# Performance work log

Hardware: AMD Instinct MI355X
Metric: run time of the kernel (lower is better)

Reference implementation:

```python
import jax, jax.numpy as jnp
import numpy as np

B, S, D, H = 1, 4096, 1024, 16
HD = D // H  # head_dim = 64
NEG = -1e9


def _rotate_half(x):
    x1, x2 = jnp.split(x, 2, axis=-1)
    return jnp.concatenate([-x2, x1], axis=-1)


def _apply_rope(x, cos, sin):
    # x: [b, s, h, hd]; cos/sin: [s, hd] -> broadcast over batch and heads
    c = cos[None, :, None, :]
    s = sin[None, :, None, :]
    return x * c + _rotate_half(x) * s


def setup_inputs() -> dict:
    key = jax.random.key(0)
    kx, kq, ko = jax.random.split(key, 3)
    x = jax.random.normal(kx, (B, S, D), dtype=jnp.float32)
    # causal additive mask (finite large-negative for safe grads)
    i = jnp.arange(S)
    attn_mask = jnp.where(i[None, :] > i[:, None], NEG, 0.0).astype(jnp.float32)[None, None]
    # standard RoPE tables
    inv_freq = 1.0 / (10000.0 ** (np.arange(0, HD, 2, dtype=np.float32) / HD))
    ang = np.arange(S, dtype=np.float32)[:, None] * inv_freq[None, :]  # [S, HD/2]
    ang = np.concatenate([ang, ang], axis=-1)  # [S, HD]
    rope_cos = jnp.asarray(np.cos(ang))
    rope_sin = jnp.asarray(np.sin(ang))
    W_qkv = jax.random.normal(kq, (D, 3 * D), dtype=jnp.float32) * (D ** -0.5)
    W_out = jax.random.normal(ko, (D, D), dtype=jnp.float32) * (D ** -0.5)
    return {"x": x, "attn_mask": attn_mask, "rope_cos": rope_cos,
            "rope_sin": rope_sin, "W_qkv": W_qkv, "W_out": W_out}


def reference(x, attn_mask, rope_cos, rope_sin, W_qkv, W_out):
    b, s, d = x.shape
    qkv = x @ W_qkv                              # [b, s, 3d]
    q, k, v = jnp.split(qkv, 3, axis=-1)
    q = q.reshape(b, s, H, HD)
    k = k.reshape(b, s, H, HD)
    v = v.reshape(b, s, H, HD)
    q = _apply_rope(q, rope_cos, rope_sin)
    k = _apply_rope(k, rope_cos, rope_sin)
    att = jnp.einsum('bqhd,bkhd->bhqk', q, k) / jnp.sqrt(jnp.float32(HD))
    att = att + attn_mask                        # additive mask broadcast [b,h,s,s]
    att = jax.nn.softmax(att, axis=-1)
    out = jnp.einsum('bhqk,bkhd->bqhd', att, v).reshape(b, s, d)
    return out @ W_out
```

## Files before the change

### kernel.cpp

```cpp
#include <hip/hip_runtime.h>


typedef __attribute__((ext_vector_type(8)))  __bf16 bf16x8;
typedef __attribute__((ext_vector_type(4)))  float  f32x4;
typedef __attribute__((ext_vector_type(16))) float  f32x16;
typedef __attribute__((ext_vector_type(8)))  unsigned short ushort8;
typedef __attribute__((ext_vector_type(4)))  unsigned int   u32x4;

#define MFMA16(a,b,c) __builtin_amdgcn_mfma_f32_16x16x32_bf16((a),(b),(c),0,0,0)
#define MFMA32(a,b,c) __builtin_amdgcn_mfma_f32_32x32x16_bf16((a),(b),(c),0,0,0)

static __device__ __forceinline__ unsigned short f2bf(float f) {
  unsigned int u = __builtin_bit_cast(unsigned int, f);
  u = (u + 0x7FFFu + ((u >> 16) & 1u)) >> 16;
  return (unsigned short)u;
}
static __device__ __forceinline__ float bf2f(unsigned short u) {
  return __builtin_bit_cast(float, (unsigned int)u << 16);
}
static __device__ __forceinline__ unsigned int cvtpk(float a, float b) {
  unsigned int r;
  asm("v_cvt_pk_bf16_f32 %0, %1, %2" : "=v"(r) : "v"(a), "v"(b));
  return r;
}
static __device__ __forceinline__ void plswap(unsigned int& a, unsigned int& b) {
#if __has_builtin(__builtin_amdgcn_permlane32_swap)
  auto r = __builtin_amdgcn_permlane32_swap(a, b, false, false);
  a = r[0]; b = r[1];
#else
  unsigned int xa = (unsigned int)__shfl_xor((int)a, 32);
  unsigned int xb = (unsigned int)__shfl_xor((int)b, 32);
  int lane = __builtin_amdgcn_mbcnt_hi(~0u, __builtin_amdgcn_mbcnt_lo(~0u, 0));
  bool hi = lane >= 32;
  a = hi ? xb : a;
  b = hi ? b : xa;
#endif
}

#if __has_builtin(__builtin_amdgcn_global_load_lds)
static __device__ __forceinline__ void STAGE16(const unsigned short* gp, const unsigned short* lp) {
  __builtin_amdgcn_global_load_lds(
      (const __attribute__((address_space(1))) void*)(unsigned long long)(uintptr_t)gp,
      (__attribute__((address_space(3))) void*)(unsigned int)(uintptr_t)lp,
      16, 0, 0);
}
static __device__ __forceinline__ void STAGE_WAIT() {  }
#else
static __device__ __forceinline__ void STAGE16(const unsigned short* gp, const unsigned short* lp) {
  unsigned int m0v = __builtin_amdgcn_readfirstlane((unsigned int)(unsigned long long)(uintptr_t)lp);
  asm volatile("s_mov_b32 m0, %0\n\tglobal_load_lds_dwordx4 %1, off"
               :: "s"(m0v), "v"(gp) : "memory");
}
static __device__ __forceinline__ void STAGE_WAIT() {
  asm volatile("s_waitcnt vmcnt(0)" ::: "memory");
}
#endif

__global__ __launch_bounds__(256) void prep_a(const float* __restrict__ x,
                                              const float* __restrict__ W_qkv,
                                              const float* __restrict__ W_out,
                                              unsigned short* __restrict__ xbf,
                                              unsigned short* __restrict__ WqkvT,
                                              unsigned short* __restrict__ WoutT) {
  __shared__ float t[32][33];
  int b = blockIdx.x, tid = threadIdx.x;
  if (b < 4096) {
    int i = (b * 256 + tid) * 4;
    float4 v = *reinterpret_cast<const float4*>(x + i);
    ushort4 u;
    u.x = f2bf(v.x); u.y = f2bf(v.y); u.z = f2bf(v.z); u.w = f2bf(v.w);
    *reinterpret_cast<ushort4*>(xbf + i) = u;
    return;
  }
  const float* W; unsigned short* WT; int R, C, cx, ry;
  if (b < 4096 + 3072) {
    int idx = b - 4096; W = W_qkv; WT = WqkvT; R = 1024; C = 3072;
    cx = idx % 96; ry = idx / 96;
  } else {
    int idx = b - 7168; W = W_out; WT = WoutT; R = 1024; C = 1024;
    cx = idx % 32; ry = idx / 32;
  }
  int c0 = cx * 32, r0 = ry * 32;
  int tx = tid & 31, ty = tid >> 5;
#pragma unroll
  for (int i = 0; i < 32; i += 8)
    t[ty + i][tx] = W[(size_t)(r0 + ty + i) * C + c0 + tx];
  __syncthreads();
#pragma unroll
  for (int i = 0; i < 32; i += 8)
    WT[(size_t)(c0 + ty + i) * R + r0 + tx] = f2bf(t[tx][ty + i]);
}

template <typename OutT>
__global__ __launch_bounds__(256) void gemm_lds(const unsigned short* __restrict__ A,
                                                const unsigned short* __restrict__ BT,
                                                OutT* __restrict__ C, int M, int N, int K) {
  __shared__ __align__(16) unsigned short As[128 * 32];
  __shared__ __align__(16) unsigned short Bs[128 * 32];
  int tid = threadIdx.x;
  int lane = tid & 63, w = tid >> 6;
  int wr = w >> 1, wc = w & 1;
  int row0 = blockIdx.y * 128, col0 = blockIdx.x * 128;
  int lr = lane & 15, lk = lane >> 4;
  int slk = (lk ^ ((lr >> 1) & 3)) * 8;
  int c0i = tid,        r0i = c0i >> 2, cs0 = ((c0i & 3) ^ ((r0i >> 1) & 3)) * 8;
  int c1i = 256 + tid,  r1i = c1i >> 2, cs1 = ((c1i & 3) ^ ((r1i >> 1) & 3)) * 8;
  const unsigned short* dA0 = &As[w * 512];
  const unsigned short* dB0 = &Bs[w * 512];
  const unsigned short* dA1 = &As[2048 + w * 512];
  const unsigned short* dB1 = &Bs[2048 + w * 512];
  const unsigned short* sA0 = A  + (size_t)(row0 + r0i) * K + cs0;
  const unsigned short* sB0 = BT + (size_t)(col0 + r0i) * K + cs0;
  const unsigned short* sA1 = A  + (size_t)(row0 + r1i) * K + cs1;
  const unsigned short* sB1 = BT + (size_t)(col0 + r1i) * K + cs1;
  f32x4 acc[4][4] = {};
  for (int k0 = 0; k0 < K; k0 += 32) {
    STAGE16(sA0 + k0, dA0);
    STAGE16(sB0 + k0, dB0);
    STAGE16(sA1 + k0, dA1);
    STAGE16(sB1 + k0, dB1);
    STAGE_WAIT();
    __syncthreads();
    bf16x8 a[4], b[4];
#pragma unroll
    for (int m = 0; m < 4; m++)
      a[m] = *reinterpret_cast<const bf16x8*>(&As[(wr * 64 + m * 16 + lr) * 32 + slk]);
#pragma unroll
    for (int n = 0; n < 4; n++)
      b[n] = *reinterpret_cast<const bf16x8*>(&Bs[(wc * 64 + n * 16 + lr) * 32 + slk]);
#pragma unroll
    for (int m = 0; m < 4; m++)
#pragma unroll
      for (int n = 0; n < 4; n++)
        acc[m][n] = MFMA16(a[m], b[n], acc[m][n]);
    __syncthreads();
  }
#pragma unroll
  for (int m = 0; m < 4; m++)
#pragma unroll
    for (int n = 0; n < 4; n++)
#pragma unroll
      for (int r = 0; r < 4; r++) {
        size_t off = (size_t)(row0 + wr * 64 + m * 16 + lk * 4 + r) * N + col0 + wc * 64 + n * 16 + lr;
        if constexpr (sizeof(OutT) == 2) C[off] = f2bf(acc[m][n][r]);
        else                             C[off] = acc[m][n][r];
      }
}

__global__ __launch_bounds__(256) void prep_b(const unsigned short* __restrict__ qkv,
                                              const float* __restrict__ cosb,
                                              const float* __restrict__ sinb,
                                              unsigned short* __restrict__ Q,
                                              unsigned short* __restrict__ K,
                                              unsigned short* __restrict__ VF) {
  __shared__ unsigned short tile[32][68];
  int b = blockIdx.x, tid = threadIdx.x;
  if (b < 2048) {
    const float QSCALE = 0.125f * 1.4426950408889634f;
    int idx = b * 256 + tid;
    int c = idx & 7, s = (idx >> 3) & 4095, h = idx >> 15;
    int d0 = c * 8;
    int base = s * 3072 + h * 64;
    ushort8 qv  = *reinterpret_cast<const ushort8*>(qkv + base + d0);
    ushort8 qv2 = *reinterpret_cast<const ushort8*>(qkv + base + (d0 ^ 32));
    ushort8 kv  = *reinterpret_cast<const ushort8*>(qkv + base + 1024 + d0);
    ushort8 kv2 = *reinterpret_cast<const ushort8*>(qkv + base + 1024 + (d0 ^ 32));
    float sign = (d0 < 32) ? -1.f : 1.f;
    const float4* cp = reinterpret_cast<const float4*>(cosb + s * 64 + d0);
    const float4* sp = reinterpret_cast<const float4*>(sinb + s * 64 + d0);
    float4 c0 = cp[0], c1 = cp[1], s0 = sp[0], s1 = sp[1];
    float co[8] = {c0.x, c0.y, c0.z, c0.w, c1.x, c1.y, c1.z, c1.w};
    float si[8] = {s0.x, s0.y, s0.z, s0.w, s1.x, s1.y, s1.z, s1.w};
    ushort8 qo, ko;
#pragma unroll
    for (int j = 0; j < 8; ++j) {
      float q = bf2f(qv[j]), q2 = bf2f(qv2[j]);
      float k = bf2f(kv[j]), k2 = bf2f(kv2[j]);
      qo[j] = f2bf((q * co[j] + sign * q2 * si[j]) * QSCALE);
      ko[j] = f2bf(k * co[j] + sign * k2 * si[j]);
    }
    *reinterpret_cast<ushort8*>(Q + (size_t)h * 262144 + (size_t)s * 64 + d0) = qo;
    int tt = s >> 5, ql = s & 31, lo = (d0 >> 3) & 1, f = d0 >> 4;
    size_t koff = (size_t)h * 262144 + (size_t)tt * 2048 + (size_t)f * 512
                + (size_t)(lo * 32 + ql) * 8;
    *reinterpret_cast<ushort8*>(K + koff) = ko;
    return;
  }
  int vb = b - 2048;
  int t = vb & 127, h = vb >> 7;
  {
    int r = tid >> 3, c8 = (tid & 7) * 8;
    *reinterpret_cast<ushort8*>(&tile[r][c8]) =
        *reinterpret_cast<const ushort8*>(qkv + (size_t)(t * 32 + r) * 3072 + 2048 + h * 64 + c8);
  }
  __syncthreads();
  int f = tid >> 6, lane = tid & 63;
  int ql = lane & 31, lo = lane >> 5;
  int sb = (f & 1) * 16 + lo * 8;
  int d  = (f >> 1) * 32 + ql;
  ushort8 v;
#pragma unroll
  for (int j = 0; j < 8; ++j) v[j] = tile[sb + j][d];
  *reinterpret_cast<ushort8*>(VF + (size_t)h * 262144 + (size_t)t * 2048
                              + (size_t)f * 512 + (size_t)lane * 8) = v;
}

__global__ __launch_bounds__(512) void flash_attn4q(const unsigned short* __restrict__ Q,
                                                    const unsigned short* __restrict__ Kf,
                                                    const unsigned short* __restrict__ Vf,
                                                    unsigned short* __restrict__ O) {
  const int S = 4096;
  __shared__ __align__(16) unsigned short sbuf[2][4][2048];
  int flat = blockIdx.x;
  int xcd = flat & 7;
  int r = flat >> 3;
  int h2 = r >> 5, rb = r & 31;
  int h = xcd * 2 + h2;
  int b = h2 ? (31 - rb) : rb;
  int nwin = (98 + b) >> 1;
  int tid = threadIdx.x;
  int lane = tid & 63, w = tid >> 6;
  int qm = w >> 1, pp = w & 1;
  int img = w >> 1, half = w & 1;
  int ql = lane & 31, lo = lane >> 5;
  const unsigned short* Qh  = Q  + (size_t)h * S * 64;
  const unsigned short* KfH = Kf + (size_t)h * S * 64;
  const unsigned short* VfH = Vf + (size_t)h * S * 64;
  const unsigned short* img_src = (img & 1) ? VfH : KfH;
  int img_dt = img >> 1;

  auto stage = [&](int nb, int win) {
    int t = 2 * win + img_dt;
    const unsigned short* src = img_src + (size_t)t * 2048 + half * 1024 + lane * 8;
    const unsigned short* dst = &sbuf[nb][img][half * 1024];
    STAGE16(src, dst);
    STAGE16(src + 512, dst + 512);
  };

  int qt = b + 32 * qm;
  int q0 = qt * 32;
  bf16x8 qf[4];
#pragma unroll
  for (int f = 0; f < 4; ++f)
    qf[f] = *reinterpret_cast<const bf16x8*>(Qh + (q0 + ql) * 64 + f * 16 + lo * 8);
  f32x16 oT0 = {}, oT1 = {};
  float l = 0.f;

  stage(0, 0);
  STAGE_WAIT();
  __syncthreads();
  int cb = 0;
  for (int win = 0; win < nwin; ++win) {
    if (win + 1 < nwin) stage(cb ^ 1, win + 1);
    int t = 2 * win + pp;
    if (t <= qt) {
      const unsigned short* kb = &sbuf[cb][2 * pp][0];
      const unsigned short* vb = &sbuf[cb][2 * pp + 1][0];
      bf16x8 k0 = *reinterpret_cast<const bf16x8*>(kb + 0 * 512 + lane * 8);
      bf16x8 k1 = *reinterpret_cast<const bf16x8*>(kb + 1 * 512 + lane * 8);
      bf16x8 k2 = *reinterpret_cast<const bf16x8*>(kb + 2 * 512 + lane * 8);
      bf16x8 k3 = *reinterpret_cast<const bf16x8*>(kb + 3 * 512 + lane * 8);
      f32x16 p = {};
      __builtin_amdgcn_s_setprio(1);
      p = MFMA32(k0, qf[0], p);
      p = MFMA32(k1, qf[1], p);
      p = MFMA32(k2, qf[2], p);
      p = MFMA32(k3, qf[3], p);
      __builtin_amdgcn_s_setprio(0);
      bf16x8 v00 = *reinterpret_cast<const bf16x8*>(vb + 0 * 512 + lane * 8);
      bf16x8 v01 = *reinterpret_cast<const bf16x8*>(vb + 1 * 512 + lane * 8);
      bf16x8 v10 = *reinterpret_cast<const bf16x8*>(vb + 2 * 512 + lane * 8);
      bf16x8 v11 = *reinterpret_cast<const bf16x8*>(vb + 3 * 512 + lane * 8);
      if (t == qt) {
#pragma unroll
        for (int r2 = 0; r2 < 16; ++r2) {
          int kvr = (r2 & 3) + 8 * (r2 >> 2) + 4 * lo;
          if (kvr > ql) p[r2] = -1e9f;
        }
      }
#pragma unroll
      for (int r2 = 0; r2 < 16; ++r2) p[r2] = __builtin_amdgcn_exp2f(p[r2]);
      {
        float s0 = (p[0] + p[1])   + (p[2] + p[3]);
        float s1 = (p[4] + p[5])   + (p[6] + p[7]);
        float s2 = (p[8] + p[9])   + (p[10] + p[11]);
        float s3 = (p[12] + p[13]) + (p[14] + p[15]);
        l += (s0 + s1) + (s2 + s3);
      }
      unsigned int A0 = cvtpk(p[0],  p[1]),  A1 = cvtpk(p[2],  p[3]);
      unsigned int B0 = cvtpk(p[4],  p[5]),  B1 = cvtpk(p[6],  p[7]);
      plswap(A0, B0); plswap(A1, B1);
      u32x4 w0 = {A0, A1, B0, B1};
      bf16x8 P0 = __builtin_bit_cast(bf16x8, w0);
      unsigned int C0 = cvtpk(p[8],  p[9]),  C1 = cvtpk(p[10], p[11]);
      unsigned int D0 = cvtpk(p[12], p[13]), D1 = cvtpk(p[14], p[15]);
      plswap(C0, D0); plswap(C1, D1);
      u32x4 w1 = {C0, C1, D0, D1};
      bf16x8 P1 = __builtin_bit_cast(bf16x8, w1);
      __builtin_amdgcn_s_setprio(1);
      oT0 = MFMA32(v00, P0, oT0);
      oT1 = MFMA32(v10, P0, oT1);
      oT0 = MFMA32(v01, P1, oT0);
      oT1 = MFMA32(v11, P1, oT1);
      __builtin_amdgcn_s_setprio(0);
    }
    STAGE_WAIT();
    __syncthreads();
    cb ^= 1;
  }

  float* fm = reinterpret_cast<float*>(&sbuf[0][0][0]);
  float* lm = fm + 2 * 64 * 33;
#pragma unroll
  for (int sub = 0; sub < 2; ++sub) {
    __syncthreads();
    if ((qm >> 1) == sub && pp == 1) {
      float* dst = fm + ((qm & 1) * 64 + lane) * 33;
#pragma unroll
      for (int r2 = 0; r2 < 16; ++r2) { dst[r2] = oT0[r2]; dst[16 + r2] = oT1[r2]; }
      lm[(qm & 1) * 64 + lane] = l;
    }
    __syncthreads();
    if ((qm >> 1) == sub && pp == 0) {
      const float* src = fm + ((qm & 1) * 64 + lane) * 33;
      float ll = l + lm[(qm & 1) * 64 + lane];
#pragma unroll
      for (int r2 = 0; r2 < 16; ++r2) {
        oT0[r2] += src[r2];
        oT1[r2] += src[16 + r2];
      }
      ll += __shfl_xor(ll, 32);
      float rl = 1.0f / ll;
      size_t obase = (size_t)(q0 + ql) * 1024 + h * 64;
#pragma unroll
      for (int r2 = 0; r2 < 16; ++r2) {
        int d = (r2 & 3) + 8 * (r2 >> 2) + 4 * lo;
        O[obase + d]      = f2bf(oT0[r2] * rl);
        O[obase + 32 + d] = f2bf(oT1[r2] * rl);
      }
    }
  }
}

extern "C" void kernel_launch(void* const* d_in, const int* in_sizes, int n_in,
                              void* d_out, int out_size, void* d_ws, size_t ws_size,
                              hipStream_t stream) {
  const float* x        = (const float*)d_in[0];
  const float* rope_cos = (const float*)d_in[2];
  const float* rope_sin = (const float*)d_in[3];
  const float* W_qkv    = (const float*)d_in[4];
  const float* W_out    = (const float*)d_in[5];
  float* out = (float*)d_out;

  char* ws = (char*)d_ws;
  const size_t MB = 1u << 20;
  unsigned short* xbf   = (unsigned short*)(ws + 0 * MB);
  unsigned short* WqkvT = (unsigned short*)(ws + 8 * MB);
  unsigned short* WoutT = (unsigned short*)(ws + 14 * MB);
  unsigned short* qkv   = (unsigned short*)(ws + 16 * MB);
  unsigned short* Qb    = (unsigned short*)(ws + 40 * MB);
  unsigned short* Kfb   = (unsigned short*)(ws + 48 * MB);
  unsigned short* Vfb   = (unsigned short*)(ws + 56 * MB);
  unsigned short* Ob    = (unsigned short*)(ws + 64 * MB);

  prep_a<<<8192, 256, 0, stream>>>(x, W_qkv, W_out, xbf, WqkvT, WoutT);

  gemm_lds<unsigned short><<<dim3(3072 / 128, 4096 / 128), 256, 0, stream>>>(
      xbf, WqkvT, qkv, 4096, 3072, 1024);

  prep_b<<<4096, 256, 0, stream>>>(qkv, rope_cos, rope_sin, Qb, Kfb, Vfb);

  flash_attn4q<<<512, 512, 0, stream>>>(Qb, Kfb, Vfb, Ob);

  gemm_lds<float><<<dim3(1024 / 128, 4096 / 128), 256, 0, stream>>>(
      Ob, WoutT, out, 4096, 1024, 1024);
}
```

Baseline: 134.3 us.

## Assign contiguous query tiles per block and stage four KV tiles per round

Each block now handles four adjacent 32-row query tiles (4g..4g+3) instead of two far-apart tiles (b and b+32), and each round stages four K/V tiles into a doubled shared buffer. Each warp then processes two KV tiles per round. This halves the number of barrier-synchronised rounds per KV span and keeps the block's query tiles close, so masked-out work is small. The cost is twice the LDS footprint, which may reduce occupancy, and a different causal load balance across blocks, since round counts now range from 1 to 32.

Result: faster. 128.6 us (-4.3%).

```diff
diff --git a/kernel.cpp b/kernel.cpp
--- a/kernel.cpp
+++ b/kernel.cpp
@@ -210,34 +210,36 @@
                                                     const unsigned short* __restrict__ Vf,
                                                     unsigned short* __restrict__ O) {
   const int S = 4096;
-  __shared__ __align__(16) unsigned short sbuf[2][4][2048];
+  __shared__ __align__(16) unsigned short sbuf[2][8][2048];
   int flat = blockIdx.x;
   int xcd = flat & 7;
-  int r = flat >> 3;
-  int h2 = r >> 5, rb = r & 31;
+  int v = flat >> 3;
+  int h2 = v >> 5, gslot = v & 31;
   int h = xcd * 2 + h2;
-  int b = h2 ? (31 - rb) : rb;
-  int nwin = (98 + b) >> 1;
+  int g = h2 ? (31 - gslot) : gslot;
+  int base4 = 4 * g;
+  int nround = g + 1;
   int tid = threadIdx.x;
   int lane = tid & 63, w = tid >> 6;
   int qm = w >> 1, pp = w & 1;
-  int img = w >> 1, half = w & 1;
   int ql = lane & 31, lo = lane >> 5;
   const unsigned short* Qh  = Q  + (size_t)h * S * 64;
   const unsigned short* KfH = Kf + (size_t)h * S * 64;
   const unsigned short* VfH = Vf + (size_t)h * S * 64;
-  const unsigned short* img_src = (img & 1) ? VfH : KfH;
-  int img_dt = img >> 1;
-
-  auto stage = [&](int nb, int win) {
-    int t = 2 * win + img_dt;
-    const unsigned short* src = img_src + (size_t)t * 2048 + half * 1024 + lane * 8;
-    const unsigned short* dst = &sbuf[nb][img][half * 1024];
-    STAGE16(src, dst);
-    STAGE16(src + 512, dst + 512);
+  const unsigned short* img_src = (w & 1) ? VfH : KfH;
+  int img_dt = w >> 1;
+
+  auto stage = [&](int nb, int rnd) {
+    int t = 4 * rnd + img_dt;
+    const unsigned short* src = img_src + (size_t)t * 2048 + lane * 8;
+    const unsigned short* dst = &sbuf[nb][w][0];
+    STAGE16(src,        dst);
+    STAGE16(src + 512,  dst + 512);
+    STAGE16(src + 1024, dst + 1024);
+    STAGE16(src + 1536, dst + 1536);
   };
 
-  int qt = b + 32 * qm;
+  int qt = base4 + qm;
   int q0 = qt * 32;
   bf16x8 qf[4];
 #pragma unroll
@@ -250,59 +252,63 @@
   STAGE_WAIT();
   __syncthreads();
   int cb = 0;
-  for (int win = 0; win < nwin; ++win) {
-    if (win + 1 < nwin) stage(cb ^ 1, win + 1);
-    int t = 2 * win + pp;
-    if (t <= qt) {
-      const unsigned short* kb = &sbuf[cb][2 * pp][0];
-      const unsigned short* vb = &sbuf[cb][2 * pp + 1][0];
-      bf16x8 k0 = *reinterpret_cast<const bf16x8*>(kb + 0 * 512 + lane * 8);
-      bf16x8 k1 = *reinterpret_cast<const bf16x8*>(kb + 1 * 512 + lane * 8);
-      bf16x8 k2 = *reinterpret_cast<const bf16x8*>(kb + 2 * 512 + lane * 8);
-      bf16x8 k3 = *reinterpret_cast<const bf16x8*>(kb + 3 * 512 + lane * 8);
-      f32x16 p = {};
-      __builtin_amdgcn_s_setprio(1);
-      p = MFMA32(k0, qf[0], p);
-      p = MFMA32(k1, qf[1], p);
-      p = MFMA32(k2, qf[2], p);
-      p = MFMA32(k3, qf[3], p);
-      __builtin_amdgcn_s_setprio(0);
-      bf16x8 v00 = *reinterpret_cast<const bf16x8*>(vb + 0 * 512 + lane * 8);
-      bf16x8 v01 = *reinterpret_cast<const bf16x8*>(vb + 1 * 512 + lane * 8);
-      bf16x8 v10 = *reinterpret_cast<const bf16x8*>(vb + 2 * 512 + lane * 8);
-      bf16x8 v11 = *reinterpret_cast<const bf16x8*>(vb + 3 * 512 + lane * 8);
-      if (t == qt) {
-#pragma unroll
-        for (int r2 = 0; r2 < 16; ++r2) {
-          int kvr = (r2 & 3) + 8 * (r2 >> 2) + 4 * lo;
-          if (kvr > ql) p[r2] = -1e9f;
+  for (int rnd = 0; rnd < nround; ++rnd) {
+    if (rnd + 1 < nround) stage(cb ^ 1, rnd + 1);
+#pragma unroll
+    for (int sub = 0; sub < 2; ++sub) {
+      int t = 4 * rnd + 2 * sub + pp;
+      if (t <= qt) {
+        int dt = 2 * sub + pp;
+        const unsigned short* kb = &sbuf[cb][2 * dt][0];
+        const unsigned short* vb = &sbuf[cb][2 * dt + 1][0];
+        bf16x8 k0 = *reinterpret_cast<const bf16x8*>(kb + 0 * 512 + lane * 8);
+        bf16x8 k1 = *reinterpret_cast<const bf16x8*>(kb + 1 * 512 + lane * 8);
+        bf16x8 k2 = *reinterpret_cast<const bf16x8*>(kb + 2 * 512 + lane * 8);
+        bf16x8 k3 = *reinterpret_cast<const bf16x8*>(kb + 3 * 512 + lane * 8);
+        f32x16 p = {};
+        __builtin_amdgcn_s_setprio(1);
+        p = MFMA32(k0, qf[0], p);
+        p = MFMA32(k1, qf[1], p);
+        p = MFMA32(k2, qf[2], p);
+        p = MFMA32(k3, qf[3], p);
+        __builtin_amdgcn_s_setprio(0);
+        bf16x8 v00 = *reinterpret_cast<const bf16x8*>(vb + 0 * 512 + lane * 8);
+        bf16x8 v01 = *reinterpret_cast<const bf16x8*>(vb + 1 * 512 + lane * 8);
+        bf16x8 v10 = *reinterpret_cast<const bf16x8*>(vb + 2 * 512 + lane * 8);
+        bf16x8 v11 = *reinterpret_cast<const bf16x8*>(vb + 3 * 512 + lane * 8);
+        if (t == qt) {
+#pragma unroll
+          for (int r2 = 0; r2 < 16; ++r2) {
+            int kvr = (r2 & 3) + 8 * (r2 >> 2) + 4 * lo;
+            if (kvr > ql) p[r2] = -1e9f;
+          }
         }
+#pragma unroll
+        for (int r2 = 0; r2 < 16; ++r2) p[r2] = __builtin_amdgcn_exp2f(p[r2]);
+        {
+          float s0 = (p[0] + p[1])   + (p[2] + p[3]);
+          float s1 = (p[4] + p[5])   + (p[6] + p[7]);
+          float s2 = (p[8] + p[9])   + (p[10] + p[11]);
+          float s3 = (p[12] + p[13]) + (p[14] + p[15]);
+          l += (s0 + s1) + (s2 + s3);
+        }
+        unsigned int A0 = cvtpk(p[0],  p[1]),  A1 = cvtpk(p[2],  p[3]);
+        unsigned int B0 = cvtpk(p[4],  p[5]),  B1 = cvtpk(p[6],  p[7]);
+        plswap(A0, B0); plswap(A1, B1);
+        u32x4 w0 = {A0, A1, B0, B1};
+        bf16x8 P0 = __builtin_bit_cast(bf16x8, w0);
+        unsigned int C0 = cvtpk(p[8],  p[9]),  C1 = cvtpk(p[10], p[11]);
+        unsigned int D0 = cvtpk(p[12], p[13]), D1 = cvtpk(p[14], p[15]);
+        plswap(C0, D0); plswap(C1, D1);
+        u32x4 w1 = {C0, C1, D0, D1};
+        bf16x8 P1 = __builtin_bit_cast(bf16x8, w1);
+        __builtin_amdgcn_s_setprio(1);
+        oT0 = MFMA32(v00, P0, oT0);
+        oT1 = MFMA32(v10, P0, oT1);
+        oT0 = MFMA32(v01, P1, oT0);
+        oT1 = MFMA32(v11, P1, oT1);
+        __builtin_amdgcn_s_setprio(0);
       }
-#pragma unroll
-      for (int r2 = 0; r2 < 16; ++r2) p[r2] = __builtin_amdgcn_exp2f(p[r2]);
-      {
-        float s0 = (p[0] + p[1])   + (p[2] + p[3]);
-        float s1 = (p[4] + p[5])   + (p[6] + p[7]);
-        float s2 = (p[8] + p[9])   + (p[10] + p[11]);
-        float s3 = (p[12] + p[13]) + (p[14] + p[15]);
-        l += (s0 + s1) + (s2 + s3);
-      }
-      unsigned int A0 = cvtpk(p[0],  p[1]),  A1 = cvtpk(p[2],  p[3]);
-      unsigned int B0 = cvtpk(p[4],  p[5]),  B1 = cvtpk(p[6],  p[7]);
-      plswap(A0, B0); plswap(A1, B1);
-      u32x4 w0 = {A0, A1, B0, B1};
-      bf16x8 P0 = __builtin_bit_cast(bf16x8, w0);
-      unsigned int C0 = cvtpk(p[8],  p[9]),  C1 = cvtpk(p[10], p[11]);
-      unsigned int D0 = cvtpk(p[12], p[13]), D1 = cvtpk(p[14], p[15]);
-      plswap(C0, D0); plswap(C1, D1);
-      u32x4 w1 = {C0, C1, D0, D1};
-      bf16x8 P1 = __builtin_bit_cast(bf16x8, w1);
-      __builtin_amdgcn_s_setprio(1);
-      oT0 = MFMA32(v00, P0, oT0);
-      oT1 = MFMA32(v10, P0, oT1);
-      oT0 = MFMA32(v01, P1, oT0);
-      oT1 = MFMA32(v11, P1, oT1);
-      __builtin_amdgcn_s_setprio(0);
     }
     STAGE_WAIT();
     __syncthreads();
```
